# Performance work log

Hardware: AMD Instinct MI355X
Metric: run time of the kernel (lower is better)

Reference implementation:

```python
import jax, jax.numpy as jnp
import numpy as np

MUL = 64          # multiplicity of every irrep block
N = 200000        # batch (e.g. edges in an equivariant GNN)
SQRT3 = 3.0 ** 0.5

# Levi-Civita tensor: real-basis Wigner 3j for 1x1->1 is eps/sqrt(6);
# e3nn's (y,z,x) ordering is a cyclic permutation so eps is unchanged.
_eps = np.zeros((3, 3, 3), dtype=np.float32)
for (i, j, k), s in {(0,1,2): 1, (1,2,0): 1, (2,0,1): 1,
                     (0,2,1): -1, (2,1,0): -1, (1,0,2): -1}.items():
    _eps[i, j, k] = s
EPS = jnp.asarray(_eps)


def setup_inputs() -> dict:
    key = jax.random.key(0)
    ks = jax.random.split(key, 7)
    return {
        "x1": jax.random.normal(ks[0], (N, 4 * MUL), jnp.float32),   # 64x0e + 64x1o
        "x2": jax.random.normal(ks[1], (N, 4), jnp.float32),          # 1x0e + 1x1o
        "w_ss_s": jax.random.normal(ks[2], (MUL, 1, MUL), jnp.float32),  # ins (0,0,0)
        "w_vv_s": jax.random.normal(ks[3], (MUL, 1, MUL), jnp.float32),  # ins (1,1,0)
        "w_sv_v": jax.random.normal(ks[4], (MUL, 1, MUL), jnp.float32),  # ins (0,1,1)
        "w_vs_v": jax.random.normal(ks[5], (MUL, 1, MUL), jnp.float32),  # ins (1,0,1)
        "w_vv_v": jax.random.normal(ks[6], (MUL, 1, MUL), jnp.float32),  # ins (1,1,1)
    }


def reference(x1, x2, w_ss_s, w_vv_s, w_sv_v, w_vs_v, w_vv_v):
    n = x1.shape[0]
    # split irreps blocks
    x1s = x1[:, :MUL]                        # [z,u]      64x0e
    x1v = x1[:, MUL:].reshape(n, MUL, 3)     # [z,u,i]    64x1o
    x2s = x2[:, :1]                          # [z,v]      1x0e
    x2v = x2[:, 1:].reshape(n, 1, 3)         # [z,v,j]    1x1o

    # e3nn path normalization (component norm, all vars/path_weights = 1):
    # alpha = sqrt(1 / sum_{ins -> same i_out} mul1*mul2)
    a0 = (1.0 / (2 * MUL)) ** 0.5            # scalar out: fan-in 64 + 64
    a1 = (1.0 / (3 * MUL)) ** 0.5            # vector out: fan-in 64 * 3

    # Wigner 3j (real basis) * sqrt(2*l_out+1)  [component normalization]:
    #   0x0->0 : 1        0x1->1, 1x0->1 : delta
    #   1x1->0 : delta/sqrt(3)     1x1->1 : eps/sqrt(2)
    out_s = a0 * (jnp.einsum('uvw,zu,zv->zw', w_ss_s, x1s, x2s)
                  + (1.0 / SQRT3) * jnp.einsum('uvw,zui,zvi->zw', w_vv_s, x1v, x2v))

    out_v = a1 * (jnp.einsum('uvw,zu,zvk->zwk', w_sv_v, x1s, x2v)
                  + jnp.einsum('uvw,zuk,zv->zwk', w_vs_v, x1v, x2s)
                  + (2.0 ** -0.5) * jnp.einsum('uvw,ijk,zui,zvj->zwk', w_vv_v, EPS, x1v, x2v))

    return jnp.concatenate([out_s, out_v.reshape(n, 3 * MUL)], axis=1)
```

## Files before the change

### kernel.cpp

```cpp
#include <hip/hip_runtime.h>

#define BLOCK 512
#define RPB   32
#define X1LD  260

__global__ __launch_bounds__(BLOCK) void tp_kernel(
    const float* __restrict__ x1, const float* __restrict__ x2,
    const float* __restrict__ w0, const float* __restrict__ w1,
    const float* __restrict__ w2, const float* __restrict__ w3,
    const float* __restrict__ w4,
    float* __restrict__ out, int n)
{
    __shared__ float lds_w[5 * 4096];
    __shared__ float lds_x1[RPB * X1LD];
    __shared__ float lds_x2[RPB * 4];

    const int t = threadIdx.x;

    {
        const float* srcs[5] = {w0, w1, w2, w3, w4};
        #pragma unroll
        for (int m = 0; m < 5; ++m) {
            const float4* s = (const float4*)srcs[m];
            float4* d = (float4*)(&lds_w[m * 4096]);
            for (int i = t; i < 1024; i += BLOCK) d[i] = s[i];
        }
    }

    const int g = t & 15;
    const int r = t >> 4;

    const int nchunks = (n + RPB - 1) / RPB;
    for (int chunk = blockIdx.x; chunk < nchunks; chunk += (int)gridDim.x) {
        const int z0 = chunk * RPB;

        for (int i = t; i < RPB * 64; i += BLOCK) {
            const int row = i >> 6;
            const int c4  = i & 63;
            const int z   = z0 + row;
            float4 v = make_float4(0.f, 0.f, 0.f, 0.f);
            if (z < n) v = *(const float4*)(x1 + (size_t)z * 256 + c4 * 4);
            *(float4*)(&lds_x1[row * X1LD + c4 * 4]) = v;
        }
        if (t < RPB * 4) {
            const int z = z0 + (t >> 2);
            lds_x2[t] = (z < n) ? x2[(size_t)z * 4 + (t & 3)] : 0.f;
        }
        __syncthreads();

        float yss[4], ysv[4], yvvs[4][3], yvs[4][3], yvvv[4][3];
        #pragma unroll
        for (int j = 0; j < 4; ++j) {
            yss[j] = 0.f; ysv[j] = 0.f;
            #pragma unroll
            for (int i = 0; i < 3; ++i) { yvvs[j][i] = 0.f; yvs[j][i] = 0.f; yvvv[j][i] = 0.f; }
        }

        const float* xr = &lds_x1[r * X1LD];
        #pragma unroll 4
        for (int u = 0; u < 64; ++u) {
            alignas(16) float wss[4], wvvs[4], wsv[4], wvs[4], wvvv[4];
            *(float4*)wss  = *(const float4*)(&lds_w[0*4096 + u*64 + 4*g]);
            *(float4*)wvvs = *(const float4*)(&lds_w[1*4096 + u*64 + 4*g]);
            *(float4*)wsv  = *(const float4*)(&lds_w[2*4096 + u*64 + 4*g]);
            *(float4*)wvs  = *(const float4*)(&lds_w[3*4096 + u*64 + 4*g]);
            *(float4*)wvvv = *(const float4*)(&lds_w[4*4096 + u*64 + 4*g]);
            const float s1  = xr[u];
            const float v1x = xr[64 + 3*u + 0];
            const float v1y = xr[64 + 3*u + 1];
            const float v1z = xr[64 + 3*u + 2];
            #pragma unroll
            for (int j = 0; j < 4; ++j) {
                yss[j]     += wss[j]  * s1;
                ysv[j]     += wsv[j]  * s1;
                yvvs[j][0] += wvvs[j] * v1x;
                yvvs[j][1] += wvvs[j] * v1y;
                yvvs[j][2] += wvvs[j] * v1z;
                yvs[j][0]  += wvs[j]  * v1x;
                yvs[j][1]  += wvs[j]  * v1y;
                yvs[j][2]  += wvs[j]  * v1z;
                yvvv[j][0] += wvvv[j] * v1x;
                yvvv[j][1] += wvvv[j] * v1y;
                yvvv[j][2] += wvvv[j] * v1z;
            }
        }

        const float a0  = 0.088388347648318447f;
        const float a1  = 0.072168783648703216f;
        const float is3 = 0.57735026918962576f;
        const float is2 = 0.70710678118654752f;
        const float s2  = lds_x2[r*4 + 0];
        const float v2x = lds_x2[r*4 + 1];
        const float v2y = lds_x2[r*4 + 2];
        const float v2z = lds_x2[r*4 + 3];
        const int z = z0 + r;
        if (z < n) {
            float* orow = out + (size_t)z * 256;
            alignas(16) float os[4];
            alignas(16) float ov[12];
            #pragma unroll
            for (int j = 0; j < 4; ++j) {
                os[j] = a0 * (yss[j]*s2 + is3*(yvvs[j][0]*v2x + yvvs[j][1]*v2y + yvvs[j][2]*v2z));
                const float cx = yvvv[j][1]*v2z - yvvv[j][2]*v2y;
                const float cy = yvvv[j][2]*v2x - yvvv[j][0]*v2z;
                const float cz = yvvv[j][0]*v2y - yvvv[j][1]*v2x;
                ov[3*j+0] = a1 * (ysv[j]*v2x + yvs[j][0]*s2 + is2*cx);
                ov[3*j+1] = a1 * (ysv[j]*v2y + yvs[j][1]*s2 + is2*cy);
                ov[3*j+2] = a1 * (ysv[j]*v2z + yvs[j][2]*s2 + is2*cz);
            }
            *(float4*)(orow + 4*g)           = *(float4*)os;
            *(float4*)(orow + 64 + 12*g + 0) = *(float4*)(ov + 0);
            *(float4*)(orow + 64 + 12*g + 4) = *(float4*)(ov + 4);
            *(float4*)(orow + 64 + 12*g + 8) = *(float4*)(ov + 8);
        }
        __syncthreads();
    }
}

extern "C" void kernel_launch(void* const* d_in, const int* in_sizes, int n_in,
                              void* d_out, int out_size, void* d_ws, size_t ws_size,
                              hipStream_t stream) {
    const float* x1 = (const float*)d_in[0];
    const float* x2 = (const float*)d_in[1];
    const float* w0 = (const float*)d_in[2];
    const float* w1 = (const float*)d_in[3];
    const float* w2 = (const float*)d_in[4];
    const float* w3 = (const float*)d_in[5];
    const float* w4 = (const float*)d_in[6];
    float* out = (float*)d_out;
    const int n = in_sizes[0] / 256;
    tp_kernel<<<256, BLOCK, 0, stream>>>(x1, x2, w0, w1, w2, w3, w4, out, n);
}
```

Measured before the change: 579.8 us.

## Register-block four rows per thread with transposed swizzled x1 tile in LDS

Each thread now computes a 4-row by 4-output tile, reading x1 as float4 column slices from a transposed, XOR-swizzled LDS tile so weights loaded from LDS are reused across four rows. The input channel dimension is processed in two halves to bound LDS use, and the persistent grid-stride loop is replaced by one block per 128 rows. This cuts LDS reads per FMA but multiplies accumulator registers, risking spills under the launch bound, and reloads all weights per block.

After: 638.5 us. 1.1x slower.

```diff
diff --git a/kernel.cpp b/kernel.cpp
--- a/kernel.cpp
+++ b/kernel.cpp
@@ -1,18 +1,20 @@
 #include <hip/hip_runtime.h>
 
 #define BLOCK 512
-#define RPB   32
-#define X1LD  260
+#define RPB   128
+#define NU    32
 
-__global__ __launch_bounds__(BLOCK) void tp_kernel(
+__device__ __forceinline__ int swz(int fl) { return ((fl >> 2) & 7) << 2; }
+
+__global__ __launch_bounds__(BLOCK, 2) void tp_kernel(
     const float* __restrict__ x1, const float* __restrict__ x2,
     const float* __restrict__ w0, const float* __restrict__ w1,
     const float* __restrict__ w2, const float* __restrict__ w3,
     const float* __restrict__ w4,
     float* __restrict__ out, int n)
 {
-    __shared__ float lds_w[5 * 4096];
-    __shared__ float lds_x1[RPB * X1LD];
+    __shared__ __align__(16) float lds_w[5 * 4096];
+    __shared__ __align__(16) float lds_x1[128 * 128];
     __shared__ float lds_x2[RPB * 4];
 
     const int t = threadIdx.x;
@@ -27,93 +29,132 @@
         }
     }
 
-    const int g = t & 15;
-    const int r = t >> 4;
+    const int g  = t & 15;
+    const int r0 = (t >> 4) * 4;
+    const int z0 = blockIdx.x * RPB;
 
-    const int nchunks = (n + RPB - 1) / RPB;
-    for (int chunk = blockIdx.x; chunk < nchunks; chunk += (int)gridDim.x) {
-        const int z0 = chunk * RPB;
+    float yss[4][4], ysv[4][4], yvvs[4][4][3], yvs[4][4][3], yvvv[4][4][3];
+    #pragma unroll
+    for (int r = 0; r < 4; ++r)
+        #pragma unroll
+        for (int j = 0; j < 4; ++j) {
+            yss[r][j] = 0.f; ysv[r][j] = 0.f;
+            #pragma unroll
+            for (int i = 0; i < 3; ++i) { yvvs[r][j][i] = 0.f; yvs[r][j][i] = 0.f; yvvv[r][j][i] = 0.f; }
+        }
 
-        for (int i = t; i < RPB * 64; i += BLOCK) {
-            const int row = i >> 6;
-            const int c4  = i & 63;
+    const float* lw0 = lds_w + 0*4096 + 4*g;
+    const float* lw1 = lds_w + 1*4096 + 4*g;
+    const float* lw2 = lds_w + 2*4096 + 4*g;
+    const float* lw3 = lds_w + 3*4096 + 4*g;
+    const float* lw4 = lds_w + 4*4096 + 4*g;
+
+    for (int h = 0; h < 2; ++h) {
+        if (h) __syncthreads();
+
+        for (int i = t; i < 128 * 32; i += BLOCK) {
+            const int row = i >> 5;
+            const int c4  = i & 31;
             const int z   = z0 + row;
             float4 v = make_float4(0.f, 0.f, 0.f, 0.f);
-            if (z < n) v = *(const float4*)(x1 + (size_t)z * 256 + c4 * 4);
-            *(float4*)(&lds_x1[row * X1LD + c4 * 4]) = v;
+            if (z < n) {
+                const float* src = (c4 < 8)
+                    ? (x1 + (size_t)z * 256 + h * NU + 4 * c4)
+                    : (x1 + (size_t)z * 256 + 64 + 96 * h + 4 * (c4 - 8));
+                v = *(const float4*)src;
+            }
+            const int fl = 4 * c4;
+            const int p  = row ^ swz(fl);
+            lds_x1[(fl + 0) * 128 + p] = v.x;
+            lds_x1[(fl + 1) * 128 + p] = v.y;
+            lds_x1[(fl + 2) * 128 + p] = v.z;
+            lds_x1[(fl + 3) * 128 + p] = v.w;
         }
-        if (t < RPB * 4) {
+        if (h == 0) {
             const int z = z0 + (t >> 2);
             lds_x2[t] = (z < n) ? x2[(size_t)z * 4 + (t & 3)] : 0.f;
         }
         __syncthreads();
 
-        float yss[4], ysv[4], yvvs[4][3], yvs[4][3], yvvv[4][3];
+        const int ub = h * NU * 64;
+        for (int uu = 0; uu < NU; ++uu) {
+            float4 wss  = *(const float4*)(lw0 + ub + uu * 64);
+            float4 wvvs = *(const float4*)(lw1 + ub + uu * 64);
+            float4 wsv  = *(const float4*)(lw2 + ub + uu * 64);
+            float4 wvs  = *(const float4*)(lw3 + ub + uu * 64);
+            float4 wvvv = *(const float4*)(lw4 + ub + uu * 64);
+
+            float4 s1  = *(const float4*)(lds_x1 + uu * 128        + (r0 ^ swz(uu)));
+            const int f0 = 32 + 3 * uu;
+            float4 v1x = *(const float4*)(lds_x1 + (f0 + 0) * 128 + (r0 ^ swz(f0 + 0)));
+            float4 v1y = *(const float4*)(lds_x1 + (f0 + 1) * 128 + (r0 ^ swz(f0 + 1)));
+            float4 v1z = *(const float4*)(lds_x1 + (f0 + 2) * 128 + (r0 ^ swz(f0 + 2)));
+
+            const float* wssf  = (const float*)&wss;
+            const float* wvvsf = (const float*)&wvvs;
+            const float* wsvf  = (const float*)&wsv;
+            const float* wvsf  = (const float*)&wvs;
+            const float* wvvvf = (const float*)&wvvv;
+            const float* s1f   = (const float*)&s1;
+            const float* v1xf  = (const float*)&v1x;
+            const float* v1yf  = (const float*)&v1y;
+            const float* v1zf  = (const float*)&v1z;
+
+            #pragma unroll
+            for (int r = 0; r < 4; ++r) {
+                const float s  = s1f[r];
+                const float vx = v1xf[r];
+                const float vy = v1yf[r];
+                const float vz = v1zf[r];
+                #pragma unroll
+                for (int j = 0; j < 4; ++j) {
+                    yss[r][j]     += wssf[j]  * s;
+                    ysv[r][j]     += wsvf[j]  * s;
+                    yvvs[r][j][0] += wvvsf[j] * vx;
+                    yvvs[r][j][1] += wvvsf[j] * vy;
+                    yvvs[r][j][2] += wvvsf[j] * vz;
+                    yvs[r][j][0]  += wvsf[j]  * vx;
+                    yvs[r][j][1]  += wvsf[j]  * vy;
+                    yvs[r][j][2]  += wvsf[j]  * vz;
+                    yvvv[r][j][0] += wvvvf[j] * vx;
+                    yvvv[r][j][1] += wvvvf[j] * vy;
+                    yvvv[r][j][2] += wvvvf[j] * vz;
+                }
+            }
+        }
+    }
+
+    const float a0  = 0.088388347648318447f;
+    const float a1  = 0.072168783648703216f;
+    const float is3 = 0.57735026918962576f;
+    const float is2 = 0.70710678118654752f;
+    #pragma unroll
+    for (int k = 0; k < 4; ++k) {
+        const int row = r0 + k;
+        const int z   = z0 + row;
+        if (z >= n) continue;
+        const float s2  = lds_x2[row * 4 + 0];
+        const float v2x = lds_x2[row * 4 + 1];
+        const float v2y = lds_x2[row * 4 + 2];
+        const float v2z = lds_x2[row * 4 + 3];
+        float* orow = out + (size_t)z * 256;
+        alignas(16) float os[4];
+        alignas(16) float ov[12];
         #pragma unroll
         for (int j = 0; j < 4; ++j) {
-            yss[j] = 0.f; ysv[j] = 0.f;
-            #pragma unroll
-            for (int i = 0; i < 3; ++i) { yvvs[j][i] = 0.f; yvs[j][i] = 0.f; yvvv[j][i] = 0.f; }
+            os[j] = a0 * (yss[k][j] * s2
+                  + is3 * (yvvs[k][j][0] * v2x + yvvs[k][j][1] * v2y + yvvs[k][j][2] * v2z));
+            const float cx = yvvv[k][j][1] * v2z - yvvv[k][j][2] * v2y;
+            const float cy = yvvv[k][j][2] * v2x - yvvv[k][j][0] * v2z;
+            const float cz = yvvv[k][j][0] * v2y - yvvv[k][j][1] * v2x;
+            ov[3*j+0] = a1 * (ysv[k][j] * v2x + yvs[k][j][0] * s2 + is2 * cx);
+            ov[3*j+1] = a1 * (ysv[k][j] * v2y + yvs[k][j][1] * s2 + is2 * cy);
+            ov[3*j+2] = a1 * (ysv[k][j] * v2z + yvs[k][j][2] * s2 + is2 * cz);
         }
-
-        const float* xr = &lds_x1[r * X1LD];
-        #pragma unroll 4
-        for (int u = 0; u < 64; ++u) {
-            alignas(16) float wss[4], wvvs[4], wsv[4], wvs[4], wvvv[4];
-            *(float4*)wss  = *(const float4*)(&lds_w[0*4096 + u*64 + 4*g]);
-            *(float4*)wvvs = *(const float4*)(&lds_w[1*4096 + u*64 + 4*g]);
-            *(float4*)wsv  = *(const float4*)(&lds_w[2*4096 + u*64 + 4*g]);
-            *(float4*)wvs  = *(const float4*)(&lds_w[3*4096 + u*64 + 4*g]);
-            *(float4*)wvvv = *(const float4*)(&lds_w[4*4096 + u*64 + 4*g]);
-            const float s1  = xr[u];
-            const float v1x = xr[64 + 3*u + 0];
-            const float v1y = xr[64 + 3*u + 1];
-            const float v1z = xr[64 + 3*u + 2];
-            #pragma unroll
-            for (int j = 0; j < 4; ++j) {
-                yss[j]     += wss[j]  * s1;
-                ysv[j]     += wsv[j]  * s1;
-                yvvs[j][0] += wvvs[j] * v1x;
-                yvvs[j][1] += wvvs[j] * v1y;
-                yvvs[j][2] += wvvs[j] * v1z;
-                yvs[j][0]  += wvs[j]  * v1x;
-                yvs[j][1]  += wvs[j]  * v1y;
-                yvs[j][2]  += wvs[j]  * v1z;
-                yvvv[j][0] += wvvv[j] * v1x;
-                yvvv[j][1] += wvvv[j] * v1y;
-                yvvv[j][2] += wvvv[j] * v1z;
-            }
-        }
-
-        const float a0  = 0.088388347648318447f;
-        const float a1  = 0.072168783648703216f;
-        const float is3 = 0.57735026918962576f;
-        const float is2 = 0.70710678118654752f;
-        const float s2  = lds_x2[r*4 + 0];
-        const float v2x = lds_x2[r*4 + 1];
-        const float v2y = lds_x2[r*4 + 2];
-        const float v2z = lds_x2[r*4 + 3];
-        const int z = z0 + r;
-        if (z < n) {
-            float* orow = out + (size_t)z * 256;
-            alignas(16) float os[4];
-            alignas(16) float ov[12];
-            #pragma unroll
-            for (int j = 0; j < 4; ++j) {
-                os[j] = a0 * (yss[j]*s2 + is3*(yvvs[j][0]*v2x + yvvs[j][1]*v2y + yvvs[j][2]*v2z));
-                const float cx = yvvv[j][1]*v2z - yvvv[j][2]*v2y;
-                const float cy = yvvv[j][2]*v2x - yvvv[j][0]*v2z;
-                const float cz = yvvv[j][0]*v2y - yvvv[j][1]*v2x;
-                ov[3*j+0] = a1 * (ysv[j]*v2x + yvs[j][0]*s2 + is2*cx);
-                ov[3*j+1] = a1 * (ysv[j]*v2y + yvs[j][1]*s2 + is2*cy);
-                ov[3*j+2] = a1 * (ysv[j]*v2z + yvs[j][2]*s2 + is2*cz);
-            }
-            *(float4*)(orow + 4*g)           = *(float4*)os;
-            *(float4*)(orow + 64 + 12*g + 0) = *(float4*)(ov + 0);
-            *(float4*)(orow + 64 + 12*g + 4) = *(float4*)(ov + 4);
-            *(float4*)(orow + 64 + 12*g + 8) = *(float4*)(ov + 8);
-        }
-        __syncthreads();
+        *(float4*)(orow + 4*g)           = *(float4*)os;
+        *(float4*)(orow + 64 + 12*g + 0) = *(float4*)(ov + 0);
+        *(float4*)(orow + 64 + 12*g + 4) = *(float4*)(ov + 4);
+        *(float4*)(orow + 64 + 12*g + 8) = *(float4*)(ov + 8);
     }
 }
 
@@ -129,5 +170,6 @@
     const float* w4 = (const float*)d_in[6];
     float* out = (float*)d_out;
     const int n = in_sizes[0] / 256;
-    tp_kernel<<<256, BLOCK, 0, stream>>>(x1, x2, w0, w1, w2, w3, w4, out, n);
+    const int nchunks = (n + RPB - 1) / RPB;
+    tp_kernel<<<nchunks, BLOCK, 0, stream>>>(x1, x2, w0, w1, w2, w3, w4, out, n);
 }
```

## Read x1 rows directly from global memory, drop LDS staging and per-chunk barriers

Applied to the files above, without the earlier changes.

Removes the LDS staging of x1/x2 tiles: each thread now loads its row's scalar and vector features straight from global memory in 8-feature chunks, and x2 is read per row at the output stage. This eliminates the per-chunk cooperative load and both __syncthreads, shrinks LDS to only the weights so more blocks can be resident, and doubles the grid. In exchange, 16 threads per row issue redundant global loads that rely on cache hits, and latency is no longer hidden by a barrier-separated load phase.

Result: slower. 622.3 us (+7.3%).

```diff
diff --git a/kernel.cpp b/kernel.cpp
--- a/kernel.cpp
+++ b/kernel.cpp
@@ -1,19 +1,16 @@
 #include <hip/hip_runtime.h>
 
 #define BLOCK 512
-#define RPB   32
-#define X1LD  260
+#define RPG   32
 
-__global__ __launch_bounds__(BLOCK) void tp_kernel(
+__global__ __launch_bounds__(BLOCK, 4) void tp_kernel(
     const float* __restrict__ x1, const float* __restrict__ x2,
     const float* __restrict__ w0, const float* __restrict__ w1,
     const float* __restrict__ w2, const float* __restrict__ w3,
     const float* __restrict__ w4,
     float* __restrict__ out, int n)
 {
-    __shared__ float lds_w[5 * 4096];
-    __shared__ float lds_x1[RPB * X1LD];
-    __shared__ float lds_x2[RPB * 4];
+    __shared__ __align__(16) float lds_w[5 * 4096];
 
     const int t = threadIdx.x;
 
@@ -26,27 +23,21 @@
             for (int i = t; i < 1024; i += BLOCK) d[i] = s[i];
         }
     }
+    __syncthreads();
 
     const int g = t & 15;
     const int r = t >> 4;
 
-    const int nchunks = (n + RPB - 1) / RPB;
-    for (int chunk = blockIdx.x; chunk < nchunks; chunk += (int)gridDim.x) {
-        const int z0 = chunk * RPB;
+    const float a0  = 0.088388347648318447f;
+    const float a1  = 0.072168783648703216f;
+    const float is3 = 0.57735026918962576f;
+    const float is2 = 0.70710678118654752f;
 
-        for (int i = t; i < RPB * 64; i += BLOCK) {
-            const int row = i >> 6;
-            const int c4  = i & 63;
-            const int z   = z0 + row;
-            float4 v = make_float4(0.f, 0.f, 0.f, 0.f);
-            if (z < n) v = *(const float4*)(x1 + (size_t)z * 256 + c4 * 4);
-            *(float4*)(&lds_x1[row * X1LD + c4 * 4]) = v;
-        }
-        if (t < RPB * 4) {
-            const int z = z0 + (t >> 2);
-            lds_x2[t] = (z < n) ? x2[(size_t)z * 4 + (t & 3)] : 0.f;
-        }
-        __syncthreads();
+    const int ngroups = (n + RPG - 1) / RPG;
+    for (int grp = blockIdx.x; grp < ngroups; grp += (int)gridDim.x) {
+        const int z   = grp * RPG + r;
+        const bool act = (z < n);
+        const float* xrow = x1 + (size_t)(act ? z : 0) * 256;
 
         float yss[4], ysv[4], yvvs[4][3], yvs[4][3], yvvv[4][3];
         #pragma unroll
@@ -56,64 +47,78 @@
             for (int i = 0; i < 3; ++i) { yvvs[j][i] = 0.f; yvs[j][i] = 0.f; yvvv[j][i] = 0.f; }
         }
 
-        const float* xr = &lds_x1[r * X1LD];
-        #pragma unroll 4
-        for (int u = 0; u < 64; ++u) {
-            alignas(16) float wss[4], wvvs[4], wsv[4], wvs[4], wvvv[4];
-            *(float4*)wss  = *(const float4*)(&lds_w[0*4096 + u*64 + 4*g]);
-            *(float4*)wvvs = *(const float4*)(&lds_w[1*4096 + u*64 + 4*g]);
-            *(float4*)wsv  = *(const float4*)(&lds_w[2*4096 + u*64 + 4*g]);
-            *(float4*)wvs  = *(const float4*)(&lds_w[3*4096 + u*64 + 4*g]);
-            *(float4*)wvvv = *(const float4*)(&lds_w[4*4096 + u*64 + 4*g]);
-            const float s1  = xr[u];
-            const float v1x = xr[64 + 3*u + 0];
-            const float v1y = xr[64 + 3*u + 1];
-            const float v1z = xr[64 + 3*u + 2];
+        #pragma unroll 1
+        for (int uc = 0; uc < 8; ++uc) {
+            alignas(16) float sarr[8];
+            alignas(16) float varr[24];
+            *(float4*)(sarr + 0) = *(const float4*)(xrow + uc * 8 + 0);
+            *(float4*)(sarr + 4) = *(const float4*)(xrow + uc * 8 + 4);
             #pragma unroll
-            for (int j = 0; j < 4; ++j) {
-                yss[j]     += wss[j]  * s1;
-                ysv[j]     += wsv[j]  * s1;
-                yvvs[j][0] += wvvs[j] * v1x;
-                yvvs[j][1] += wvvs[j] * v1y;
-                yvvs[j][2] += wvvs[j] * v1z;
-                yvs[j][0]  += wvs[j]  * v1x;
-                yvs[j][1]  += wvs[j]  * v1y;
-                yvs[j][2]  += wvs[j]  * v1z;
-                yvvv[j][0] += wvvv[j] * v1x;
-                yvvv[j][1] += wvvv[j] * v1y;
-                yvvv[j][2] += wvvv[j] * v1z;
+            for (int k = 0; k < 6; ++k)
+                *(float4*)(varr + 4 * k) = *(const float4*)(xrow + 64 + uc * 24 + 4 * k);
+
+            #pragma unroll
+            for (int q = 0; q < 8; ++q) {
+                const int u = uc * 8 + q;
+                const float4 wss  = *(const float4*)(&lds_w[0 * 4096 + u * 64 + 4 * g]);
+                const float4 wvvs = *(const float4*)(&lds_w[1 * 4096 + u * 64 + 4 * g]);
+                const float4 wsv  = *(const float4*)(&lds_w[2 * 4096 + u * 64 + 4 * g]);
+                const float4 wvs  = *(const float4*)(&lds_w[3 * 4096 + u * 64 + 4 * g]);
+                const float4 wvvv = *(const float4*)(&lds_w[4 * 4096 + u * 64 + 4 * g]);
+
+                const float s  = sarr[q];
+                const float vx = varr[3 * q + 0];
+                const float vy = varr[3 * q + 1];
+                const float vz = varr[3 * q + 2];
+
+                const float* wssf  = (const float*)&wss;
+                const float* wvvsf = (const float*)&wvvs;
+                const float* wsvf  = (const float*)&wsv;
+                const float* wvsf  = (const float*)&wvs;
+                const float* wvvvf = (const float*)&wvvv;
+
+                #pragma unroll
+                for (int j = 0; j < 4; ++j) {
+                    yss[j]     += wssf[j]  * s;
+                    ysv[j]     += wsvf[j]  * s;
+                    yvvs[j][0] += wvvsf[j] * vx;
+                    yvvs[j][1] += wvvsf[j] * vy;
+                    yvvs[j][2] += wvvsf[j] * vz;
+                    yvs[j][0]  += wvsf[j]  * vx;
+                    yvs[j][1]  += wvsf[j]  * vy;
+                    yvs[j][2]  += wvsf[j]  * vz;
+                    yvvv[j][0] += wvvvf[j] * vx;
+                    yvvv[j][1] += wvvvf[j] * vy;
+                    yvvv[j][2] += wvvvf[j] * vz;
+                }
             }
         }
 
-        const float a0  = 0.088388347648318447f;
-        const float a1  = 0.072168783648703216f;
-        const float is3 = 0.57735026918962576f;
-        const float is2 = 0.70710678118654752f;
-        const float s2  = lds_x2[r*4 + 0];
-        const float v2x = lds_x2[r*4 + 1];
-        const float v2y = lds_x2[r*4 + 2];
-        const float v2z = lds_x2[r*4 + 3];
-        const int z = z0 + r;
-        if (z < n) {
+        if (act) {
+            const float4 x2v = *(const float4*)(x2 + (size_t)z * 4);
+            const float s2  = x2v.x;
+            const float v2x = x2v.y;
+            const float v2y = x2v.z;
+            const float v2z = x2v.w;
             float* orow = out + (size_t)z * 256;
             alignas(16) float os[4];
             alignas(16) float ov[12];
             #pragma unroll
             for (int j = 0; j < 4; ++j) {
-                os[j] = a0 * (yss[j]*s2 + is3*(yvvs[j][0]*v2x + yvvs[j][1]*v2y + yvvs[j][2]*v2z));
-                const float cx = yvvv[j][1]*v2z - yvvv[j][2]*v2y;
-                const float cy = yvvv[j][2]*v2x - yvvv[j][0]*v2z;
-                const float cz = yvvv[j][0]*v2y - yvvv[j][1]*v2x;
-                ov[3*j+0] = a1 * (ysv[j]*v2x + yvs[j][0]*s2 + is2*cx);
-                ov[3*j+1] = a1 * (ysv[j]*v2y + yvs[j][1]*s2 + is2*cy);
-                ov[3*j+2] = a1 * (ysv[j]*v2z + yvs[j][2]*s2 + is2*cz);
+                os[j] = a0 * (yss[j] * s2
+                      + is3 * (yvvs[j][0] * v2x + yvvs[j][1] * v2y + yvvs[j][2] * v2z));
+                const float cx = yvvv[j][1] * v2z - yvvv[j][2] * v2y;
+                const float cy = yvvv[j][2] * v2x - yvvv[j][0] * v2z;
+                const float cz = yvvv[j][0] * v2y - yvvv[j][1] * v2x;
+                ov[3*j+0] = a1 * (ysv[j] * v2x + yvs[j][0] * s2 + is2 * cx);
+                ov[3*j+1] = a1 * (ysv[j] * v2y + yvs[j][1] * s2 + is2 * cy);
+                ov[3*j+2] = a1 * (ysv[j] * v2z + yvs[j][2] * s2 + is2 * cz);
             }
             *(float4*)(orow + 4*g)           = *(float4*)os;
             *(float4*)(orow + 64 + 12*g + 0) = *(float4*)(ov + 0);
             *(float4*)(orow + 64 + 12*g + 4) = *(float4*)(ov + 4);
             *(float4*)(orow + 64 + 12*g + 8) = *(float4*)(ov + 8);
         }
-        __syncthreads();
     }
 }
 
@@ -129,5 +134,5 @@
     const float* w4 = (const float*)d_in[6];
     float* out = (float*)d_out;
     const int n = in_sizes[0] / 256;
-    tp_kernel<<<256, BLOCK, 0, stream>>>(x1, x2, w0, w1, w2, w3, w4, out, n);
+    tp_kernel<<<512, BLOCK, 0, stream>>>(x1, x2, w0, w1, w2, w3, w4, out, n);
 }
```
